# Kernel tuning notes

Hardware: AMD Instinct MI355X
Metric: run time of the kernel (lower is better)

Reference implementation:

```python
import jax, jax.numpy as jnp
import numpy as np

H = 128; N = 64; B = 128; L = 3; F = 7; E = 64; LAT = 128
NEG = -1e9

def _ln(x, g, b, eps=1e-5):
    m = jnp.mean(x, axis=-1, keepdims=True)
    v = jnp.mean((x - m) ** 2, axis=-1, keepdims=True)
    return (x - m) / jnp.sqrt(v + eps) * g + b

def setup_inputs() -> dict:
    key = jax.random.key(0)
    ks = iter(jax.random.split(key, 64))
    def w(shape, s=0.05):
        return (jax.random.normal(next(ks), shape, dtype=jnp.float32) * s)
    inp = {}
    inp['battery_features'] = jax.random.normal(next(ks), (B, F), dtype=jnp.float32)
    inp['material_embeddings'] = jax.random.normal(next(ks), (B, N, E), dtype=jnp.float32)
    inp['node_mask'] = (jax.random.uniform(next(ks), (B, N)) > 0.2).astype(jnp.float32)
    # material encoder: Linear(E,H), LN, ReLU, Linear(H,H), LN, ReLU
    inp['enc_W1'] = w((E, H)); inp['enc_b1'] = jnp.zeros((H,))
    inp['enc_g1'] = jnp.ones((H,)); inp['enc_B1'] = jnp.zeros((H,))
    inp['enc_W2'] = w((H, H)); inp['enc_b2'] = jnp.zeros((H,))
    inp['enc_g2'] = jnp.ones((H,)); inp['enc_B2'] = jnp.zeros((H,))
    # per-layer GATv2 params (stacked over L layers)
    inp['Wq'] = w((L, H, H)); inp['bq'] = jnp.zeros((L, H))
    inp['Wk'] = w((L, H, H)); inp['bk'] = jnp.zeros((L, H))
    inp['Wv'] = w((L, H, H)); inp['bv'] = jnp.zeros((L, H))
    inp['We1'] = w((L, 2 * H, H)); inp['be1'] = jnp.zeros((L, H))
    inp['We2'] = w((L, H)); inp['be2'] = jnp.zeros((L,))
    inp['Wo'] = w((L, H, H)); inp['bo'] = jnp.zeros((L, H))
    inp['o_g'] = jnp.ones((L, H)); inp['o_B'] = jnp.zeros((L, H))
    # legacy decoder: Linear(F+H,H), LN, ReLU, Linear(H,LAT), LN, ReLU, Linear(LAT,F)
    inp['dW1'] = w((F + H, H)); inp['db1'] = jnp.zeros((H,))
    inp['dg1'] = jnp.ones((H,)); inp['dB1'] = jnp.zeros((H,))
    inp['dW2'] = w((H, LAT)); inp['db2'] = jnp.zeros((LAT,))
    inp['dg2'] = jnp.ones((LAT,)); inp['dB2'] = jnp.zeros((LAT,))
    inp['dW3'] = w((LAT, F)); inp['db3'] = jnp.zeros((F,))
    return inp

def reference(battery_features, material_embeddings, node_mask,
              enc_W1, enc_b1, enc_g1, enc_B1, enc_W2, enc_b2, enc_g2, enc_B2,
              Wq, bq, Wk, bk, Wv, bv, We1, be1, We2, be2, Wo, bo, o_g, o_B,
              dW1, db1, dg1, dB1, dW2, db2, dg2, dB2, dW3, db3):
    # material encoder (dropout=0 / eval)
    x = material_embeddings  # [B,N,E]
    h = jax.nn.relu(_ln(x @ enc_W1 + enc_b1, enc_g1, enc_B1))
    h = jax.nn.relu(_ln(h @ enc_W2 + enc_b2, enc_g2, enc_B2))
    x = h * node_mask[..., None]  # [B,N,H]
    mask2d = node_mask[:, :, None] * node_mask[:, None, :]  # [B,N,N]
    nlayers = Wq.shape[0]
    for l in range(nlayers):
        q = x @ Wq[l] + bq[l]
        k = x @ Wk[l] + bk[l]
        v = x @ Wv[l] + bv[l]
        # edge MLP on concat(q_i, k_j): split first linear, avoid concat materialization
        hq = q @ We1[l, :H]          # [B,N,H]
        hk = k @ We1[l, H:]          # [B,N,H]
        eh = jax.nn.relu(hq[:, :, None, :] + hk[:, None, :, :] + be1[l])  # [B,N,N,H]
        scores = jnp.einsum('bijh,h->bij', eh, We2[l]) + be2[l]
        scores = jnp.where(mask2d > 0, scores, NEG)
        attn = jax.nn.softmax(scores, axis=-1) * mask2d
        agg = jnp.einsum('bij,bjh->bih', attn, v)
        x = jax.nn.relu(_ln(agg @ Wo[l] + bo[l], o_g[l], o_B[l]))
        x = x * node_mask[..., None]
    # masked mean pooling
    denom = jnp.clip(jnp.sum(node_mask, axis=1, keepdims=True), 1.0, None)
    pooled = jnp.sum(x * node_mask[..., None], axis=1) / denom  # [B,H]
    d = jnp.concatenate([battery_features, pooled], axis=-1)
    z = jax.nn.relu(_ln(d @ dW1 + db1, dg1, dB1))
    z = jax.nn.relu(_ln(z @ dW2 + db2, dg2, dB2))
    return z @ dW3 + db3  # [B,F] predicted properties
```

## Files before the change

### kernel.cpp

```cpp
#include <hip/hip_runtime.h>


constexpr float EPS = 1e-5f;
constexpr float NEGI = -1e9f;

typedef __bf16 bf16x8 __attribute__((ext_vector_type(8)));
typedef float floatx4 __attribute__((ext_vector_type(4)));
typedef _Float16 h2 __attribute__((ext_vector_type(2)));
union U32H2 { unsigned int u; h2 h; };

__device__ __forceinline__ unsigned int pkh2(float a, float b) {
  U32H2 u; u.h[0] = (_Float16)a; u.h[1] = (_Float16)b; return u.u;
}
__device__ __forceinline__ float fdot2h(h2 a, h2 b, float c) {
#if __has_builtin(__builtin_amdgcn_fdot2)
  return __builtin_amdgcn_fdot2(a, b, c, false);
#else
  return c + (float)a[0] * (float)b[0] + (float)a[1] * (float)b[1];
#endif
}
__device__ __forceinline__ bf16x8 cvt8(const float* p) {
  float t[8];
  *(float4*)t = *(const float4*)p;
  *(float4*)(t + 4) = *(const float4*)(p + 4);
  bf16x8 r;
#pragma unroll
  for (int j = 0; j < 8; ++j) r[j] = (__bf16)t[j];
  return r;
}

__global__ __launch_bounds__(256) void prep_kernel(
    const float* __restrict__ Wq, const float* __restrict__ bq,
    const float* __restrict__ Wk, const float* __restrict__ bk,
    const float* __restrict__ bv, const float* __restrict__ We1,
    const float* __restrict__ be1,
    const float* __restrict__ eW1, const float* __restrict__ eW2,
    const float* __restrict__ Wv, const float* __restrict__ Wo,
    const float* __restrict__ We2,
    __bf16* __restrict__ w1pk, __bf16* __restrict__ w2pk,
    __bf16* __restrict__ wcatpk, __bf16* __restrict__ wopk,
    float* __restrict__ bcat, unsigned int* __restrict__ w2hg) {
  int tid = threadIdx.x, blk = blockIdx.x;
  if (blk < 48) {
    __shared__ float sB[128 * 16];
    __shared__ float sF[128 * 17];
    int jb = blk >> 3, cc = blk & 7;
    int l = jb >> 1, w = jb & 1;
    const float* A = (w ? Wk : Wq) + l * 16384;
    const float* Bm = We1 + l * 32768 + w * 16384;
    int c0 = cc * 16;
    for (int idx = tid; idx < 2048; idx += 256) {
      int m = idx >> 4, c = idx & 15;
      sB[idx] = Bm[m * 128 + c0 + c];
    }
    __syncthreads();
    int r = tid >> 1, c8 = (tid & 1) * 8;
    float acc[8] = {};
    const float4* A4 = (const float4*)(A + r * 128);
#pragma unroll 8
    for (int k4 = 0; k4 < 32; ++k4) {
      float4 a = A4[k4];
      float av[4] = {a.x, a.y, a.z, a.w};
#pragma unroll
      for (int kk = 0; kk < 4; ++kk)
#pragma unroll
        for (int c = 0; c < 8; ++c)
          acc[c] = fmaf(av[kk], sB[(k4 * 4 + kk) * 16 + c8 + c], acc[c]);
    }
    for (int c = 0; c < 8; ++c) sF[r * 17 + c8 + c] = acc[c];
    __syncthreads();
    int kc = tid >> 6, ln = tid & 63;
    int k0 = kc * 32 + (ln >> 4) * 8, n = ln & 15;
    bf16x8 pk;
#pragma unroll
    for (int j = 0; j < 8; ++j) pk[j] = (__bf16)sF[(k0 + j) * 17 + n];
    int ntg = 8 + w * 8 + cc;
    *((bf16x8*)(wcatpk + l * 49152) + (ntg * 4 + kc) * 64 + ln) = pk;
  } else if (blk < 56) {
    int job = blk - 48;
    const float* src;
    __bf16* dst;
    int KCH = 4;
    if (job == 0) { src = eW1; dst = w1pk; KCH = 2; }
    else if (job == 1) { src = eW2; dst = w2pk; }
    else if (job < 5) { int l = job - 2; src = Wv + l * 16384; dst = wcatpk + l * 49152; }
    else { int l = job - 5; src = Wo + l * 16384; dst = wopk + l * 16384; }
    for (int s = tid; s < 8 * KCH * 64; s += 256) {
      int ln = s & 63, q = s >> 6;
      int kc = q % KCH, nt = q / KCH;
      int k0 = kc * 32 + (ln >> 4) * 8, n = nt * 16 + (ln & 15);
      bf16x8 pk;
#pragma unroll
      for (int j = 0; j < 8; ++j) pk[j] = (__bf16)src[(k0 + j) * 128 + n];
      *((bf16x8*)dst + (nt * KCH + kc) * 64 + ln) = pk;
    }
  } else {
    for (int idx = tid; idx < 3 * 384; idx += 256) {
      int l = idx / 384, c = idx % 384;
      float val;
      if (c < 128) {
        val = bv[l * 128 + c];
      } else if (c < 256) {
        int cc2 = c - 128;
        float s = 0.f;
        for (int k = 0; k < 128; ++k) s += bq[l * 128 + k] * We1[l * 32768 + k * 128 + cc2];
        val = s;
      } else {
        int cc2 = c - 256;
        float s = be1[l * 128 + cc2];
        for (int k = 0; k < 128; ++k) s += bk[l * 128 + k] * We1[l * 32768 + 16384 + k * 128 + cc2];
        val = s;
      }
      bcat[l * 384 + c] = val;
    }
    for (int idx = tid; idx < 192; idx += 256) {
      int l = idx >> 6, c = idx & 63;
      w2hg[l * 64 + c] = pkh2(We2[l * 128 + 2 * c], We2[l * 128 + 2 * c + 1]);
    }
  }
}

__device__ __forceinline__ void ln16(float* sT, __bf16* SX, const float* __restrict__ g,
                                     const float* __restrict__ be, float mreg,
                                     int i0, int tid, int mode) {
  int r = tid >> 4, c0 = tid & 15;
  const float* base = sT + r * 132;
  float s = 0.f, q = 0.f;
#pragma unroll
  for (int k = 0; k < 8; ++k) { float v = base[c0 + k * 16]; s += v; q += v * v; }
  s += __shfl_xor(s, 1); s += __shfl_xor(s, 2); s += __shfl_xor(s, 4); s += __shfl_xor(s, 8);
  q += __shfl_xor(q, 1); q += __shfl_xor(q, 2); q += __shfl_xor(q, 4); q += __shfl_xor(q, 8);
  float m = s * (1.f / 128.f);
  float rs = rsqrtf(fmaxf(q * (1.f / 128.f) - m * m, 0.f) + EPS);
  float mk = (mode >= 1) ? __shfl(mreg, i0 + r) : 1.f;
  int c8 = c0 * 8;
  float vals[8];
  *(float4*)vals = *(const float4*)(base + c8);
  *(float4*)(vals + 4) = *(const float4*)(base + c8 + 4);
#pragma unroll
  for (int k = 0; k < 8; ++k)
    vals[k] = fmaxf((vals[k] - m) * rs * g[c8 + k] + be[c8 + k], 0.f) * mk;
  if (mode < 2) {
    bf16x8 pk;
#pragma unroll
    for (int k = 0; k < 8; ++k) pk[k] = (__bf16)vals[k];
    ((bf16x8*)SX)[(c8 >> 5) * 64 + ((c8 >> 3) & 3) * 16 + r] = pk;
  } else {
    *(float4*)(sT + r * 132 + c8) = *(float4*)vals;
    *(float4*)(sT + r * 132 + c8 + 4) = *(float4*)(vals + 4);
  }
}

__device__ __forceinline__ void qkv_tail(
    const __bf16* SX, float* sTv,
    int b, int i0, const __bf16* __restrict__ wc, const float* __restrict__ bc,
    unsigned int* __restrict__ hqg_o, unsigned int* __restrict__ hkT_o,
    __bf16* __restrict__ vpk_o, int tid) {
  int lane = tid & 63, wv = tid >> 6, quad = lane >> 4, cl = lane & 15;
  bf16x8 ax[4];
#pragma unroll
  for (int kc = 0; kc < 4; ++kc) ax[kc] = ((const bf16x8*)SX)[kc * 64 + lane];
  floatx4 acc[6];
#pragma unroll
  for (int n = 0; n < 6; ++n) acc[n] = 0;
#pragma unroll
  for (int kc = 0; kc < 4; ++kc)
#pragma unroll
    for (int n = 0; n < 6; ++n) {
      bf16x8 bw = ((const bf16x8*)wc)[((wv + n * 4) * 4 + kc) * 64 + lane];
      if (n < 2)
        acc[n] = __builtin_amdgcn_mfma_f32_16x16x32_bf16(ax[kc], bw, acc[n], 0, 0, 0);
      else
        acc[n] = __builtin_amdgcn_mfma_f32_16x16x32_bf16(bw, ax[kc], acc[n], 0, 0, 0);
    }
#pragma unroll
  for (int n = 0; n < 6; ++n) {
    int g = wv + n * 4;
    if (n < 2) {
      int coll = g * 16 + cl;
      float bb = bc[coll];
#pragma unroll
      for (int r = 0; r < 4; ++r) sTv[(quad * 4 + r) * 132 + coll] = acc[n][r] + bb;
    } else if (n < 4) {
      int hb = (g - 8) * 16 + quad * 4;
      float4 bb4 = *(const float4*)(bc + 128 + hb);
      uint2 o;
      o.x = pkh2(acc[n][0] + bb4.x, acc[n][1] + bb4.y);
      o.y = pkh2(acc[n][2] + bb4.z, acc[n][3] + bb4.w);
      *(uint2*)(hqg_o + (b * 64 + i0 + cl) * 64 + (hb >> 1)) = o;
    } else {
      int hb = (g - 16) * 16 + quad * 4;
      float4 bb4 = *(const float4*)(bc + 256 + hb);
      hkT_o[b * 4096 + (hb >> 1) * 64 + i0 + cl] =
          pkh2(acc[n][0] + bb4.x, acc[n][1] + bb4.y);
      hkT_o[b * 4096 + ((hb >> 1) + 1) * 64 + i0 + cl] =
          pkh2(acc[n][2] + bb4.z, acc[n][3] + bb4.w);
    }
  }
  __syncthreads();
  {
    int nt = tid >> 5, dq = (tid >> 4) & 1, c2 = tid & 15;
    int kcv = i0 >> 5, qg = ((i0 & 31) >> 3) + dq;
    bf16x8 pk;
#pragma unroll
    for (int jj = 0; jj < 8; ++jj) pk[jj] = (__bf16)sTv[(dq * 8 + jj) * 132 + nt * 16 + c2];
    ((bf16x8*)vpk_o)[b * 1024 + (nt * 2 + kcv) * 64 + qg * 16 + c2] = pk;
  }
}

__global__ __launch_bounds__(256) void enc_qkv_kernel(
    const float* __restrict__ emb, const float* __restrict__ mask,
    const float* __restrict__ eb1, const float* __restrict__ eg1, const float* __restrict__ eB1,
    const float* __restrict__ eb2, const float* __restrict__ eg2, const float* __restrict__ eB2,
    const __bf16* __restrict__ w1pk, const __bf16* __restrict__ w2pk,
    const __bf16* __restrict__ wcat0, const float* __restrict__ bcat0,
    unsigned int* __restrict__ hqg, unsigned int* __restrict__ hkT,
    __bf16* __restrict__ vpk) {
  __shared__ __align__(16) __bf16 SX[2048];
  __shared__ __align__(16) float sTv[16 * 132];
  float* sT = sTv;
  int tid = threadIdx.x, blk = blockIdx.x;
  int lane = tid & 63, wv = tid >> 6, quad = lane >> 4, cl = lane & 15;
  int b = blk >> 2, i0 = (blk & 3) * 16;
  float mreg = mask[b * 64 + lane];

  {
    bf16x8 a1[2];
#pragma unroll
    for (int kc = 0; kc < 2; ++kc)
      a1[kc] = cvt8(emb + (b * 64 + i0 + cl) * 64 + kc * 32 + quad * 8);
    floatx4 acc[2];
    acc[0] = 0; acc[1] = 0;
#pragma unroll
    for (int kc = 0; kc < 2; ++kc)
#pragma unroll
      for (int n = 0; n < 2; ++n) {
        bf16x8 bw = ((const bf16x8*)w1pk)[((wv + n * 4) * 2 + kc) * 64 + lane];
        acc[n] = __builtin_amdgcn_mfma_f32_16x16x32_bf16(a1[kc], bw, acc[n], 0, 0, 0);
      }
#pragma unroll
    for (int n = 0; n < 2; ++n) {
      int col = (wv + n * 4) * 16 + cl;
      float bb = eb1[col];
#pragma unroll
      for (int r = 0; r < 4; ++r) sT[(quad * 4 + r) * 132 + col] = acc[n][r] + bb;
    }
  }
  __syncthreads();
  ln16(sT, SX, eg1, eB1, mreg, i0, tid, 0);
  __syncthreads();
  {
    bf16x8 a2[4];
#pragma unroll
    for (int kc = 0; kc < 4; ++kc) a2[kc] = ((const bf16x8*)SX)[kc * 64 + lane];
    floatx4 acc[2];
    acc[0] = 0; acc[1] = 0;
#pragma unroll
    for (int kc = 0; kc < 4; ++kc)
#pragma unroll
      for (int n = 0; n < 2; ++n) {
        bf16x8 bw = ((const bf16x8*)w2pk)[((wv + n * 4) * 4 + kc) * 64 + lane];
        acc[n] = __builtin_amdgcn_mfma_f32_16x16x32_bf16(a2[kc], bw, acc[n], 0, 0, 0);
      }
    __syncthreads();
#pragma unroll
    for (int n = 0; n < 2; ++n) {
      int col = (wv + n * 4) * 16 + cl;
      float bb = eb2[col];
#pragma unroll
      for (int r = 0; r < 4; ++r) sT[(quad * 4 + r) * 132 + col] = acc[n][r] + bb;
    }
  }
  __syncthreads();
  ln16(sT, SX, eg2, eB2, mreg, i0, tid, 1);
  __syncthreads();
  qkv_tail(SX, sTv, b, i0, wcat0, bcat0, hqg, hkT, vpk, tid);
}

template <bool LAST>
__global__ __launch_bounds__(256, 4) void layer_kernel(
    const unsigned int* __restrict__ hq_in, const unsigned int* __restrict__ hkT_in,
    const __bf16* __restrict__ vp_in, const float* __restrict__ mask,
    const unsigned int* __restrict__ w2hl, const float* __restrict__ be2p,
    const __bf16* __restrict__ wopk_l, const float* __restrict__ bo_l,
    const float* __restrict__ og_l, const float* __restrict__ oB_l,
    const __bf16* __restrict__ wcat_n, const float* __restrict__ bcat_n,
    unsigned int* __restrict__ hq_out, unsigned int* __restrict__ hkT_out,
    __bf16* __restrict__ vpk_out, float* __restrict__ poolp) {
  __shared__ __align__(16) __bf16 pA[1024];
  __shared__ __align__(16) __bf16 pA2[2048];
  __shared__ __align__(16) __bf16 SX[2048];
  __shared__ __align__(16) float sTv[16 * 132];
  float* sT = sTv;
  int tid = threadIdx.x, blk = blockIdx.x;
  int lane = tid & 63, wv = tid >> 6, quad = lane >> 4, cl = lane & 15;
  int b = blk >> 2, i0 = (blk & 3) * 16;
  float mreg = mask[b * 64 + lane];

  {
    int j = lane;
    const unsigned int* hkg = hkT_in + b * 4096;
    int wvu = __builtin_amdgcn_readfirstlane(wv);
    const unsigned int* hqr = hq_in + (b * 64 + i0 + wvu * 4) * 64;
    float accs[4] = {0.f, 0.f, 0.f, 0.f};
    h2 hz = {(_Float16)0.0f, (_Float16)0.0f};
#pragma unroll 4
    for (int c4 = 0; c4 < 16; ++c4) {
      int hp0 = c4 * 4;
      uint4 w2v = *(const uint4*)(w2hl + hp0);
      uint4 hkv;
      hkv.x = hkg[(hp0 + 0) * 64 + j];
      hkv.y = hkg[(hp0 + 1) * 64 + j];
      hkv.z = hkg[(hp0 + 2) * 64 + j];
      hkv.w = hkg[(hp0 + 3) * 64 + j];
#pragma unroll
      for (int il = 0; il < 4; ++il) {
        uint4 hqv = *(const uint4*)(hqr + il * 64 + hp0);
        U32H2 ha, hb, wc2;
        h2 s2;
        ha.u = hqv.x; hb.u = hkv.x; wc2.u = w2v.x;
        s2 = __builtin_elementwise_max(ha.h + hb.h, hz);
        accs[il] = fdot2h(s2, wc2.h, accs[il]);
        ha.u = hqv.y; hb.u = hkv.y; wc2.u = w2v.y;
        s2 = __builtin_elementwise_max(ha.h + hb.h, hz);
        accs[il] = fdot2h(s2, wc2.h, accs[il]);
        ha.u = hqv.z; hb.u = hkv.z; wc2.u = w2v.z;
        s2 = __builtin_elementwise_max(ha.h + hb.h, hz);
        accs[il] = fdot2h(s2, wc2.h, accs[il]);
        ha.u = hqv.w; hb.u = hkv.w; wc2.u = w2v.w;
        s2 = __builtin_elementwise_max(ha.h + hb.h, hz);
        accs[il] = fdot2h(s2, wc2.h, accs[il]);
      }
    }
    float be2v = be2p[0];
    float mj = mreg;
#pragma unroll
    for (int kk = 0; kk < 4; ++kk) {
      int il = wv * 4 + kk;
      float mi = __shfl(mreg, i0 + il);
      float m2 = mi * mj;
      float sc = (m2 > 0.f) ? accs[kk] + be2v : NEGI;
      float mx = sc;
#pragma unroll
      for (int off = 32; off >= 1; off >>= 1) mx = fmaxf(mx, __shfl_xor(mx, off));
      float p = __expf(sc - mx);
      float sm = p;
#pragma unroll
      for (int off = 32; off >= 1; off >>= 1) sm += __shfl_xor(sm, off);
      float a = p / sm * m2;
      pA[((j >> 5) * 64 + ((j >> 3) & 3) * 16 + il) * 8 + (j & 7)] = (__bf16)a;
    }
  }
  __syncthreads();

  {
    bf16x8 aat[2];
#pragma unroll
    for (int kc = 0; kc < 2; ++kc) aat[kc] = ((const bf16x8*)pA)[kc * 64 + lane];
    floatx4 acc[2];
    acc[0] = 0; acc[1] = 0;
#pragma unroll
    for (int kc = 0; kc < 2; ++kc)
#pragma unroll
      for (int n = 0; n < 2; ++n) {
        bf16x8 bw = ((const bf16x8*)vp_in)[b * 1024 + ((wv + n * 4) * 2 + kc) * 64 + lane];
        acc[n] = __builtin_amdgcn_mfma_f32_16x16x32_bf16(aat[kc], bw, acc[n], 0, 0, 0);
      }
#pragma unroll
    for (int n = 0; n < 2; ++n) {
      int hcol = (wv + n * 4) * 16 + cl;
#pragma unroll
      for (int r = 0; r < 4; ++r) {
        int i = quad * 4 + r;
        pA2[((hcol >> 5) * 64 + ((hcol >> 3) & 3) * 16 + i) * 8 + (hcol & 7)] =
            (__bf16)acc[n][r];
      }
    }
  }
  __syncthreads();

  {
    bf16x8 ag[4];
#pragma unroll
    for (int kc = 0; kc < 4; ++kc) ag[kc] = ((const bf16x8*)pA2)[kc * 64 + lane];
    floatx4 acc[2];
    acc[0] = 0; acc[1] = 0;
#pragma unroll
    for (int kc = 0; kc < 4; ++kc)
#pragma unroll
      for (int n = 0; n < 2; ++n) {
        bf16x8 bw = ((const bf16x8*)wopk_l)[((wv + n * 4) * 4 + kc) * 64 + lane];
        acc[n] = __builtin_amdgcn_mfma_f32_16x16x32_bf16(ag[kc], bw, acc[n], 0, 0, 0);
      }
#pragma unroll
    for (int n = 0; n < 2; ++n) {
      int col = (wv + n * 4) * 16 + cl;
      float bb = bo_l[col];
#pragma unroll
      for (int r = 0; r < 4; ++r) sT[(quad * 4 + r) * 132 + col] = acc[n][r] + bb;
    }
  }
  __syncthreads();
  ln16(sT, SX, og_l, oB_l, mreg, i0, tid, LAST ? 2 : 1);
  __syncthreads();
  if (!LAST) {
    qkv_tail(SX, sTv, b, i0, wcat_n, bcat_n, hq_out, hkT_out, vpk_out, tid);
  } else {
    if (tid < 128) {
      float s = 0.f;
#pragma unroll
      for (int r = 0; r < 16; ++r) s += sT[r * 132 + tid];
      poolp[blk * 128 + tid] = s;
    }
  }
}

__global__ __launch_bounds__(256) void dec_kernel(
    const float* __restrict__ bfeat, const float* __restrict__ poolp,
    const float* __restrict__ mask,
    const float* __restrict__ dW1, const float* __restrict__ db1,
    const float* __restrict__ dg1, const float* __restrict__ dB1,
    const float* __restrict__ dW2, const float* __restrict__ db2,
    const float* __restrict__ dg2, const float* __restrict__ dB2,
    const float* __restrict__ dW3, const float* __restrict__ db3,
    float* __restrict__ out) {
  __shared__ float sd[144];
  __shared__ float part[8 * 128];
  __shared__ float szz[128];
  __shared__ float red[4];
  int b = blockIdx.x, tid = threadIdx.x;
  int lane = tid & 63;
  float mreg = mask[b * 64 + lane];
  float den = mreg;
#pragma unroll
  for (int off = 32; off >= 1; off >>= 1) den += __shfl_xor(den, off);
  den = fmaxf(den, 1.f);
  if (tid < 7) sd[tid] = bfeat[b * 7 + tid];
  if (tid < 128) {
    float pooled = poolp[(b * 4 + 0) * 128 + tid] + poolp[(b * 4 + 1) * 128 + tid] +
                   poolp[(b * 4 + 2) * 128 + tid] + poolp[(b * 4 + 3) * 128 + tid];
    sd[7 + tid] = pooled / den;
  }
  __syncthreads();

  int t4 = (tid & 31) * 4, g8 = tid >> 5;
  {
    float4 zp = {0.f, 0.f, 0.f, 0.f};
#pragma unroll 4
    for (int k = g8; k < 135; k += 8) {
      float s = sd[k];
      float4 w = *(const float4*)(dW1 + k * 128 + t4);
      zp.x = fmaf(s, w.x, zp.x);
      zp.y = fmaf(s, w.y, zp.y);
      zp.z = fmaf(s, w.z, zp.z);
      zp.w = fmaf(s, w.w, zp.w);
    }
    *(float4*)(part + g8 * 128 + t4) = zp;
  }
  __syncthreads();
  int t = tid & 127;
  {
    float z = db1[t];
#pragma unroll
    for (int w = 0; w < 8; ++w) z += part[w * 128 + t];
    float s = z, q = z * z;
#pragma unroll
    for (int off = 32; off >= 1; off >>= 1) { s += __shfl_xor(s, off); q += __shfl_xor(q, off); }
    if (tid < 128 && lane == 0) { red[(tid >> 6) * 2] = s; red[(tid >> 6) * 2 + 1] = q; }
    __syncthreads();
    float S = red[0] + red[2], Q = red[1] + red[3];
    float m = S * (1.f / 128.f);
    float rs = rsqrtf(fmaxf(Q * (1.f / 128.f) - m * m, 0.f) + EPS);
    z = fmaxf((z - m) * rs * dg1[t] + dB1[t], 0.f);
    __syncthreads();
    if (tid < 128) szz[t] = z;
  }
  __syncthreads();
  {
    float4 zp = {0.f, 0.f, 0.f, 0.f};
#pragma unroll 4
    for (int k = g8; k < 128; k += 8) {
      float s = szz[k];
      float4 w = *(const float4*)(dW2 + k * 128 + t4);
      zp.x = fmaf(s, w.x, zp.x);
      zp.y = fmaf(s, w.y, zp.y);
      zp.z = fmaf(s, w.z, zp.z);
      zp.w = fmaf(s, w.w, zp.w);
    }
    *(float4*)(part + g8 * 128 + t4) = zp;
  }
  __syncthreads();
  {
    float y = db2[t];
#pragma unroll
    for (int w = 0; w < 8; ++w) y += part[w * 128 + t];
    float s = y, q = y * y;
#pragma unroll
    for (int off = 32; off >= 1; off >>= 1) { s += __shfl_xor(s, off); q += __shfl_xor(q, off); }
    if (tid < 128 && lane == 0) { red[(tid >> 6) * 2] = s; red[(tid >> 6) * 2 + 1] = q; }
    __syncthreads();
    float S = red[0] + red[2], Q = red[1] + red[3];
    float m = S * (1.f / 128.f);
    float rs = rsqrtf(fmaxf(Q * (1.f / 128.f) - m * m, 0.f) + EPS);
    y = fmaxf((y - m) * rs * dg2[t] + dB2[t], 0.f);
    __syncthreads();
    if (tid < 128) szz[t] = y;
  }
  __syncthreads();
  if (tid < 112) {
    int t7 = tid % 7, kg = tid / 7;
    float o = 0.f;
#pragma unroll
    for (int k = 0; k < 8; ++k)
      o = fmaf(szz[kg * 8 + k], dW3[(kg * 8 + k) * 7 + t7], o);
    part[kg * 7 + t7] = o;
  }
  __syncthreads();
  if (tid < 7) {
    float o = db3[tid];
#pragma unroll
    for (int kg = 0; kg < 16; ++kg) o += part[kg * 7 + tid];
    out[b * 7 + tid] = o;
  }
}

extern "C" void kernel_launch(void* const* d_in, const int* in_sizes, int n_in,
                              void* d_out, int out_size, void* d_ws, size_t ws_size,
                              hipStream_t stream) {
  const float* bf   = (const float*)d_in[0];
  const float* emb  = (const float*)d_in[1];
  const float* mask = (const float*)d_in[2];
  const float* eW1 = (const float*)d_in[3];
  const float* eb1 = (const float*)d_in[4];
  const float* eg1 = (const float*)d_in[5];
  const float* eB1 = (const float*)d_in[6];
  const float* eW2 = (const float*)d_in[7];
  const float* eb2 = (const float*)d_in[8];
  const float* eg2 = (const float*)d_in[9];
  const float* eB2 = (const float*)d_in[10];
  const float* Wq = (const float*)d_in[11];
  const float* bq = (const float*)d_in[12];
  const float* Wk = (const float*)d_in[13];
  const float* bk = (const float*)d_in[14];
  const float* Wv = (const float*)d_in[15];
  const float* bv = (const float*)d_in[16];
  const float* We1 = (const float*)d_in[17];
  const float* be1 = (const float*)d_in[18];
  const float* We2 = (const float*)d_in[19];
  const float* be2 = (const float*)d_in[20];
  const float* Wo = (const float*)d_in[21];
  const float* bo = (const float*)d_in[22];
  const float* og = (const float*)d_in[23];
  const float* oB = (const float*)d_in[24];
  const float* dW1 = (const float*)d_in[25];
  const float* db1 = (const float*)d_in[26];
  const float* dg1 = (const float*)d_in[27];
  const float* dB1 = (const float*)d_in[28];
  const float* dW2 = (const float*)d_in[29];
  const float* db2 = (const float*)d_in[30];
  const float* dg2 = (const float*)d_in[31];
  const float* dB2 = (const float*)d_in[32];
  const float* dW3 = (const float*)d_in[33];
  const float* db3 = (const float*)d_in[34];
  float* out = (float*)d_out;

  char* ws = (char*)d_ws;
  float* bcat = (float*)(ws + 1024);
  unsigned int* w2hg = (unsigned int*)(ws + 6144);
  __bf16* w1pk   = (__bf16*)(ws + 8192);
  __bf16* w2pk   = (__bf16*)(ws + 24576);
  __bf16* wcatpk = (__bf16*)(ws + 57344);
  __bf16* wopk   = (__bf16*)(ws + 352256);
  unsigned int* hqg = (unsigned int*)(ws + 524288);
  unsigned int* hkT = (unsigned int*)(ws + 4718592);
  __bf16* vpk = (__bf16*)(ws + 8912896);
  float* poolp = (float*)(ws + 13107200);

  prep_kernel<<<57, 256, 0, stream>>>(Wq, bq, Wk, bk, bv, We1, be1,
                                      eW1, eW2, Wv, Wo, We2,
                                      w1pk, w2pk, wcatpk, wopk, bcat, w2hg);
  enc_qkv_kernel<<<512, 256, 0, stream>>>(emb, mask, eb1, eg1, eB1, eb2, eg2, eB2,
                                          w1pk, w2pk, wcatpk, bcat, hqg, hkT, vpk);
  layer_kernel<false><<<512, 256, 0, stream>>>(
      hqg, hkT, vpk, mask, w2hg, be2, wopk, bo, og, oB,
      wcatpk + 49152, bcat + 384,
      hqg + 524288, hkT + 524288, vpk + 1048576, nullptr);
  layer_kernel<false><<<512, 256, 0, stream>>>(
      hqg + 524288, hkT + 524288, vpk + 1048576, mask, w2hg + 64, be2 + 1,
      wopk + 16384, bo + 128, og + 128, oB + 128,
      wcatpk + 2 * 49152, bcat + 2 * 384,
      hqg, hkT, vpk, nullptr);
  layer_kernel<true><<<512, 256, 0, stream>>>(
      hqg, hkT, vpk, mask, w2hg + 128, be2 + 2,
      wopk + 2 * 16384, bo + 256, og + 256, oB + 256,
      nullptr, nullptr, nullptr, nullptr, nullptr, poolp);
  dec_kernel<<<128, 256, 0, stream>>>(bf, poolp, mask, dW1, db1, dg1, dB1,
                                      dW2, db2, dg2, dB2, dW3, db3, out);
}
```

Before: 195.3 us.

## Fold output projection Wo into value projection Wv to drop per-layer GEMM

Precomputes Wv·Wo per layer in the prep kernel and folds bv·Wo + bo into the value bias, so the packed value weights already produce output-projected values. The layer kernel then skips the aggregate-times-Wo MFMA stage, its LDS staging buffer and one barrier, writing the attention aggregate straight into the layer-norm input. This is exact because attention rows sum to one for unmasked nodes, and masked rows are zeroed after the norm anyway. The cost is extra work in the one-time prep kernel and a possible precision change from rounding the fused weight product to bf16.

```diff
diff --git a/kernel.cpp b/kernel.cpp
--- a/kernel.cpp
+++ b/kernel.cpp
@@ -32,22 +32,22 @@
 __global__ __launch_bounds__(256) void prep_kernel(
     const float* __restrict__ Wq, const float* __restrict__ bq,
     const float* __restrict__ Wk, const float* __restrict__ bk,
-    const float* __restrict__ bv, const float* __restrict__ We1,
-    const float* __restrict__ be1,
+    const float* __restrict__ Wv, const float* __restrict__ bv,
+    const float* __restrict__ We1, const float* __restrict__ be1,
     const float* __restrict__ eW1, const float* __restrict__ eW2,
-    const float* __restrict__ Wv, const float* __restrict__ Wo,
+    const float* __restrict__ Wo, const float* __restrict__ bo,
     const float* __restrict__ We2,
     __bf16* __restrict__ w1pk, __bf16* __restrict__ w2pk,
-    __bf16* __restrict__ wcatpk, __bf16* __restrict__ wopk,
+    __bf16* __restrict__ wcatpk,
     float* __restrict__ bcat, unsigned int* __restrict__ w2hg) {
   int tid = threadIdx.x, blk = blockIdx.x;
-  if (blk < 48) {
+  if (blk < 72) {
     __shared__ float sB[128 * 16];
     __shared__ float sF[128 * 17];
     int jb = blk >> 3, cc = blk & 7;
-    int l = jb >> 1, w = jb & 1;
-    const float* A = (w ? Wk : Wq) + l * 16384;
-    const float* Bm = We1 + l * 32768 + w * 16384;
+    int l = jb / 3, w = jb % 3;
+    const float* A = (w == 0 ? Wq : (w == 1 ? Wk : Wv)) + l * 16384;
+    const float* Bm = (w < 2) ? (We1 + l * 32768 + w * 16384) : (Wo + l * 16384);
     int c0 = cc * 16;
     for (int idx = tid; idx < 2048; idx += 256) {
       int m = idx >> 4, c = idx & 15;
@@ -74,17 +74,13 @@
     bf16x8 pk;
 #pragma unroll
     for (int j = 0; j < 8; ++j) pk[j] = (__bf16)sF[(k0 + j) * 17 + n];
-    int ntg = 8 + w * 8 + cc;
+    int ntg = (w == 2) ? cc : (8 + w * 8 + cc);
     *((bf16x8*)(wcatpk + l * 49152) + (ntg * 4 + kc) * 64 + ln) = pk;
-  } else if (blk < 56) {
-    int job = blk - 48;
-    const float* src;
-    __bf16* dst;
-    int KCH = 4;
-    if (job == 0) { src = eW1; dst = w1pk; KCH = 2; }
-    else if (job == 1) { src = eW2; dst = w2pk; }
-    else if (job < 5) { int l = job - 2; src = Wv + l * 16384; dst = wcatpk + l * 49152; }
-    else { int l = job - 5; src = Wo + l * 16384; dst = wopk + l * 16384; }
+  } else if (blk < 74) {
+    int job = blk - 72;
+    const float* src = job ? eW2 : eW1;
+    __bf16* dst = job ? w2pk : w1pk;
+    int KCH = job ? 4 : 2;
     for (int s = tid; s < 8 * KCH * 64; s += 256) {
       int ln = s & 63, q = s >> 6;
       int kc = q % KCH, nt = q / KCH;
@@ -99,7 +95,9 @@
       int l = idx / 384, c = idx % 384;
       float val;
       if (c < 128) {
-        val = bv[l * 128 + c];
+        float s = bo[l * 128 + c];
+        for (int k = 0; k < 128; ++k) s += bv[l * 128 + k] * Wo[l * 16384 + k * 128 + c];
+        val = s;
       } else if (c < 256) {
         int cc2 = c - 128;
         float s = 0.f;
@@ -282,13 +280,11 @@
     const unsigned int* __restrict__ hq_in, const unsigned int* __restrict__ hkT_in,
     const __bf16* __restrict__ vp_in, const float* __restrict__ mask,
     const unsigned int* __restrict__ w2hl, const float* __restrict__ be2p,
-    const __bf16* __restrict__ wopk_l, const float* __restrict__ bo_l,
     const float* __restrict__ og_l, const float* __restrict__ oB_l,
     const __bf16* __restrict__ wcat_n, const float* __restrict__ bcat_n,
     unsigned int* __restrict__ hq_out, unsigned int* __restrict__ hkT_out,
     __bf16* __restrict__ vpk_out, float* __restrict__ poolp) {
   __shared__ __align__(16) __bf16 pA[1024];
-  __shared__ __align__(16) __bf16 pA2[2048];
   __shared__ __align__(16) __bf16 SX[2048];
   __shared__ __align__(16) float sTv[16 * 132];
   float* sT = sTv;
@@ -368,36 +364,9 @@
       }
 #pragma unroll
     for (int n = 0; n < 2; ++n) {
-      int hcol = (wv + n * 4) * 16 + cl;
-#pragma unroll
-      for (int r = 0; r < 4; ++r) {
-        int i = quad * 4 + r;
-        pA2[((hcol >> 5) * 64 + ((hcol >> 3) & 3) * 16 + i) * 8 + (hcol & 7)] =
-            (__bf16)acc[n][r];
-      }
-    }
-  }
-  __syncthreads();
-
-  {
-    bf16x8 ag[4];
-#pragma unroll
-    for (int kc = 0; kc < 4; ++kc) ag[kc] = ((const bf16x8*)pA2)[kc * 64 + lane];
-    floatx4 acc[2];
-    acc[0] = 0; acc[1] = 0;
-#pragma unroll
-    for (int kc = 0; kc < 4; ++kc)
-#pragma unroll
-      for (int n = 0; n < 2; ++n) {
-        bf16x8 bw = ((const bf16x8*)wopk_l)[((wv + n * 4) * 4 + kc) * 64 + lane];
-        acc[n] = __builtin_amdgcn_mfma_f32_16x16x32_bf16(ag[kc], bw, acc[n], 0, 0, 0);
-      }
-#pragma unroll
-    for (int n = 0; n < 2; ++n) {
       int col = (wv + n * 4) * 16 + cl;
-      float bb = bo_l[col];
-#pragma unroll
-      for (int r = 0; r < 4; ++r) sT[(quad * 4 + r) * 132 + col] = acc[n][r] + bb;
+#pragma unroll
+      for (int r = 0; r < 4; ++r) sT[(quad * 4 + r) * 132 + col] = acc[n][r];
     }
   }
   __syncthreads();
@@ -570,29 +539,28 @@
   __bf16* w1pk   = (__bf16*)(ws + 8192);
   __bf16* w2pk   = (__bf16*)(ws + 24576);
   __bf16* wcatpk = (__bf16*)(ws + 57344);
-  __bf16* wopk   = (__bf16*)(ws + 352256);
   unsigned int* hqg = (unsigned int*)(ws + 524288);
   unsigned int* hkT = (unsigned int*)(ws + 4718592);
   __bf16* vpk = (__bf16*)(ws + 8912896);
   float* poolp = (float*)(ws + 13107200);
 
-  prep_kernel<<<57, 256, 0, stream>>>(Wq, bq, Wk, bk, bv, We1, be1,
-                                      eW1, eW2, Wv, Wo, We2,
-                                      w1pk, w2pk, wcatpk, wopk, bcat, w2hg);
+  prep_kernel<<<75, 256, 0, stream>>>(Wq, bq, Wk, bk, Wv, bv, We1, be1,
+                                      eW1, eW2, Wo, bo, We2,
+                                      w1pk, w2pk, wcatpk, bcat, w2hg);
   enc_qkv_kernel<<<512, 256, 0, stream>>>(emb, mask, eb1, eg1, eB1, eb2, eg2, eB2,
                                           w1pk, w2pk, wcatpk, bcat, hqg, hkT, vpk);
   layer_kernel<false><<<512, 256, 0, stream>>>(
-      hqg, hkT, vpk, mask, w2hg, be2, wopk, bo, og, oB,
+      hqg, hkT, vpk, mask, w2hg, be2, og, oB,
       wcatpk + 49152, bcat + 384,
       hqg + 524288, hkT + 524288, vpk + 1048576, nullptr);
   layer_kernel<false><<<512, 256, 0, stream>>>(
       hqg + 524288, hkT + 524288, vpk + 1048576, mask, w2hg + 64, be2 + 1,
-      wopk + 16384, bo + 128, og + 128, oB + 128,
+      og + 128, oB + 128,
       wcatpk + 2 * 49152, bcat + 2 * 384,
       hqg, hkT, vpk, nullptr);
   layer_kernel<true><<<512, 256, 0, stream>>>(
       hqg, hkT, vpk, mask, w2hg + 128, be2 + 2,
-      wopk + 2 * 16384, bo + 256, og + 256, oB + 256,
+      og + 256, oB + 256,
       nullptr, nullptr, nullptr, nullptr, nullptr, poolp);
   dec_kernel<<<128, 256, 0, stream>>>(bf, poolp, mask, dW1, db1, dg1, dB1,
                                       dW2, db2, dg2, dB2, dW3, db3, out);
```

Result: no change. 198.3 us (+1.5%).
